# Performance work log

Measured on AMD Instinct MI355X. Metric: run time of the kernel, lower is better.

## Reference

```python
import jax, jax.numpy as jnp
import numpy as np

NUM_HEADS = 16
ROPE_THETA = 10000.0


def _rope_tables(T, head_dim, dtype=jnp.float32):
    # Standard rotate-half RoPE tables: [T, head_dim]
    half = head_dim // 2
    inv_freq = 1.0 / (ROPE_THETA ** (jnp.arange(0, half, dtype=jnp.float32) / half))
    ang = jnp.arange(T, dtype=jnp.float32)[:, None] * inv_freq[None, :]  # [T, half]
    cos = jnp.concatenate([jnp.cos(ang), jnp.cos(ang)], axis=-1).astype(dtype)
    sin = jnp.concatenate([jnp.sin(ang), jnp.sin(ang)], axis=-1).astype(dtype)
    return cos, sin


def _apply_rope(x, cos, sin):
    # x: [B, T, H, D]; cos/sin: [T, D]
    D = x.shape[-1]
    x1, x2 = x[..., : D // 2], x[..., D // 2 :]
    rotated = jnp.concatenate([-x2, x1], axis=-1)
    return x * cos[None, :, None, :] + rotated * sin[None, :, None, :]


def setup_inputs() -> dict:
    key = jax.random.key(0)
    k1, k2, k3 = jax.random.split(key, 3)
    B, T, C = 4, 2048, 2048
    x = jax.random.normal(k1, (B, T, C), dtype=jnp.float32)
    w_attn = jax.random.normal(k2, (C, 3 * C), dtype=jnp.float32) * 0.02
    w_proj = jax.random.normal(k3, (C, C), dtype=jnp.float32) * 0.02
    return {"x": x, "w_attn": w_attn, "w_proj": w_proj}


def reference(x, w_attn, w_proj):
    B, T, C = x.shape
    H = NUM_HEADS
    D = C // H

    qkv = x @ w_attn                         # [B, T, 3C]
    q, k, v = jnp.split(qkv, 3, axis=-1)
    q = q.reshape(B, T, H, D)
    k = k.reshape(B, T, H, D)
    v = v.reshape(B, T, H, D)

    cos, sin = _rope_tables(T, D, x.dtype)
    q = _apply_rope(q, cos, sin)
    k = _apply_rope(k, cos, sin)

    # causal SDPA, heads-first layout [B, H, T, D]
    scale = 1.0 / jnp.sqrt(jnp.asarray(D, dtype=x.dtype))
    scores = jnp.einsum("bqhd,bkhd->bhqk", q, k) * scale  # [B, H, T, T]
    causal = jnp.tril(jnp.ones((T, T), dtype=bool))
    scores = jnp.where(causal[None, None], scores, jnp.finfo(scores.dtype).min)
    attn = jax.nn.softmax(scores, axis=-1)
    y = jnp.einsum("bhqk,bkhd->bqhd", attn, v).reshape(B, T, C)
    return y @ w_proj
```

## Files before the change

kernel.cpp:

```cpp
#include <hip/hip_runtime.h>

typedef __bf16 bf16;
typedef __bf16 bf16x8 __attribute__((ext_vector_type(8)));
typedef __bf16 bf16x4 __attribute__((ext_vector_type(4)));
typedef __bf16 bf16x2 __attribute__((ext_vector_type(2)));
typedef float floatx4 __attribute__((ext_vector_type(4)));
typedef float floatx16 __attribute__((ext_vector_type(16)));

#define NB 4
#define NT 2048
#define NC 2048
#define NH 16
#define ND 128
#define QKS 4096

__device__ __forceinline__ void load_lds16(const void* gptr, void* ldsptr) {
  __builtin_amdgcn_global_load_lds(
      (const __attribute__((address_space(1))) unsigned int*)gptr,
      (__attribute__((address_space(3))) unsigned int*)ldsptr, 16, 0, 0);
}

__device__ __forceinline__ unsigned pack2(float a, float b) {
  bf16x2 v;
  v[0] = (bf16)a; v[1] = (bf16)b;
  return __builtin_bit_cast(unsigned, v);
}

__global__ __launch_bounds__(256) void cast_f32_bf16(const float* __restrict__ in,
                                                     bf16* __restrict__ out) {
  const int i = blockIdx.x * 256 + threadIdx.x;
  const float4 v = ((const float4*)in)[i];
  bf16x4 o;
  o[0] = (bf16)v.x; o[1] = (bf16)v.y; o[2] = (bf16)v.z; o[3] = (bf16)v.w;
  ((bf16x4*)out)[i] = o;
}

__global__ __launch_bounds__(256) void transpose_cast(const float* __restrict__ in,
                                                      bf16* __restrict__ out,
                                                      int R, int Cc) {
  __shared__ float tile[128][65];
  const int r0 = blockIdx.y * 128, c0 = blockIdx.x * 64;
  const int rr = threadIdx.x >> 6, cc = threadIdx.x & 63;
#pragma unroll
  for (int i = 0; i < 32; ++i)
    tile[rr + i * 4][cc] = in[(size_t)(r0 + rr + i * 4) * Cc + c0 + cc];
  __syncthreads();
  const int rv = threadIdx.x & 63, halfr = (threadIdx.x >> 6) & 1, crh = threadIdx.x >> 7;
#pragma unroll
  for (int i = 0; i < 32; ++i) {
    const int cr = crh * 32 + i;
    out[(size_t)(c0 + cr) * R + r0 + halfr * 64 + rv] = (bf16)tile[halfr * 64 + rv][cr];
  }
}

__device__ __forceinline__ void stage_half(bf16* lds, const bf16* __restrict__ g,
                                           int row0, int k0, int h, int K,
                                           int w, int l) {
#pragma unroll
  for (int i = 0; i < 2; ++i) {
    const int fb = h * 1024 + w * 128 + i * 64;
    const int f = fb + l;
    const int r = f >> 3, cs = f & 7, c = cs ^ (r & 7);
    load_lds16(g + (size_t)(row0 + r) * K + k0 + c * 8, lds + fb * 8);
  }
}

template <int EPI, typename OutT>
__global__ __launch_bounds__(512, 2) void gemm_bt(const bf16* __restrict__ A,
                                                  const bf16* __restrict__ Bt,
                                                  OutT* __restrict__ C,
                                                  bf16* __restrict__ qk,
                                                  bf16* __restrict__ vt,
                                                  int M, int N, int K, int NTX) {
  __shared__ bf16 smem[65536];
  __shared__ float invf_s[64];
  const int tid = threadIdx.x;
  const int w = tid >> 6, l = tid & 63, quad = l >> 4, l16 = l & 15;
  const int wm = w >> 2, wn = w & 3;

  const int cpx = gridDim.x >> 3;
  const int orig = blockIdx.x;
  const int wgid = (orig & 7) * cpx + (orig >> 3);
  const int per = 8 * NTX;
  const int band = wgid / per, rem = wgid - band * per;
  const int by = band * 8 + (rem & 7), bx = rem >> 3;
  const int m0 = by * 256, n0 = bx * 256;

  if (EPI == 1 && tid < 64)
    invf_s[tid] = exp2f(-(float)tid * 0.20762050593046014f);

  const int KT = K >> 6;

  const int sw = l16 & 7;
  const int aoff0 = (wm * 128 + l16) * 64 + ((0 + quad) ^ sw) * 8;
  const int aoff1 = (wm * 128 + l16) * 64 + ((4 + quad) ^ sw) * 8;
  const int boff0 = (wn * 64 + l16) * 64 + ((0 + quad) ^ sw) * 8;
  const int boff1 = (wn * 64 + l16) * 64 + ((4 + quad) ^ sw) * 8;

  const floatx4 fzero = {0.f, 0.f, 0.f, 0.f};
  floatx4 acc[8][4];
#pragma unroll
  for (int i = 0; i < 8; ++i)
#pragma unroll
    for (int j = 0; j < 4; ++j) acc[i][j] = fzero;

  bf16x8 af[2][2][2];
  bf16x8 bfr[2][4];

  {
    stage_half(smem, A, m0, 0, 0, K, w, l);
    stage_half(smem, A, m0, 0, 1, K, w, l);
    stage_half(smem + 16384, Bt, n0, 0, 0, K, w, l);
    stage_half(smem + 16384, Bt, n0, 0, 1, K, w, l);
    asm volatile("s_waitcnt vmcnt(0)" ::: "memory");
    __builtin_amdgcn_sched_barrier(0);
    __builtin_amdgcn_s_barrier();
    __builtin_amdgcn_sched_barrier(0);
#pragma unroll
    for (int mr = 0; mr < 2; ++mr) {
      af[0][mr][0] = *(const bf16x8*)(smem + aoff0 + mr * 1024);
      af[0][mr][1] = *(const bf16x8*)(smem + aoff1 + mr * 1024);
    }
#pragma unroll
    for (int ni = 0; ni < 4; ++ni) {
      bfr[0][ni] = *(const bf16x8*)(smem + 16384 + boff0 + ni * 1024);
      bfr[1][ni] = *(const bf16x8*)(smem + 16384 + boff1 + ni * 1024);
    }
  }

#pragma unroll 1
  for (int t = 0; t < KT; ++t) {
    bf16* cur = smem + ((t & 1) << 15);
    bf16* nxt = smem + (((t + 1) & 1) << 15);

#pragma unroll
    for (int p = 0; p < 4; ++p) {
      if (p < 3) {
#pragma unroll
        for (int mr = 0; mr < 2; ++mr) {
          af[(p + 1) & 1][mr][0] =
              *(const bf16x8*)(cur + aoff0 + ((p + 1) * 32 + mr * 16) * 64);
          af[(p + 1) & 1][mr][1] =
              *(const bf16x8*)(cur + aoff1 + ((p + 1) * 32 + mr * 16) * 64);
        }
        if (p == 0 && t + 1 < KT) {
          stage_half(nxt + 16384, Bt, n0, (t + 1) * 64, 0, K, w, l);
          stage_half(nxt + 16384, Bt, n0, (t + 1) * 64, 1, K, w, l);
        }
        if (p == 1 && t + 1 < KT) {
          stage_half(nxt, A, m0, (t + 1) * 64, 0, K, w, l);
          stage_half(nxt, A, m0, (t + 1) * 64, 1, K, w, l);
        }
        __builtin_amdgcn_sched_barrier(0);
        __builtin_amdgcn_s_barrier();
        asm volatile("s_waitcnt lgkmcnt(4)" ::: "memory");
        __builtin_amdgcn_sched_barrier(0);
      } else {
        asm volatile("s_waitcnt vmcnt(0)" ::: "memory");
        __builtin_amdgcn_sched_barrier(0);
        __builtin_amdgcn_s_barrier();
        __builtin_amdgcn_sched_barrier(0);
        if (t + 1 < KT) {
#pragma unroll
          for (int mr = 0; mr < 2; ++mr) {
            af[0][mr][0] = *(const bf16x8*)(nxt + aoff0 + mr * 1024);
            af[0][mr][1] = *(const bf16x8*)(nxt + aoff1 + mr * 1024);
          }
          asm volatile("s_waitcnt lgkmcnt(4)" ::: "memory");
        } else {
          asm volatile("s_waitcnt lgkmcnt(0)" ::: "memory");
        }
        __builtin_amdgcn_sched_barrier(0);
      }

      __builtin_amdgcn_s_setprio(1);
#pragma unroll
      for (int mr = 0; mr < 2; ++mr)
#pragma unroll
        for (int ks = 0; ks < 2; ++ks)
#pragma unroll
          for (int ni = 0; ni < 4; ++ni)
            acc[p * 2 + mr][ni] = __builtin_amdgcn_mfma_f32_16x16x32_bf16(
                af[p & 1][mr][ks], bfr[ks][ni], acc[p * 2 + mr][ni], 0, 0, 0);
      __builtin_amdgcn_s_setprio(0);
      __builtin_amdgcn_sched_barrier(0);

      if (p == 3 && t + 1 < KT) {
#pragma unroll
        for (int ni = 0; ni < 4; ++ni) {
          bfr[0][ni] = *(const bf16x8*)(nxt + 16384 + boff0 + ni * 1024);
          bfr[1][ni] = *(const bf16x8*)(nxt + 16384 + boff1 + ni * 1024);
        }
        __builtin_amdgcn_sched_barrier(0);
      }
      __builtin_amdgcn_s_barrier();
    }
  }

  if constexpr (EPI == 0) {
#pragma unroll
    for (int mi = 0; mi < 8; ++mi)
#pragma unroll
      for (int ni = 0; ni < 4; ++ni) {
        const int row = m0 + wm * 128 + mi * 16 + quad * 4;
        const int col = n0 + wn * 64 + ni * 16 + l16;
#pragma unroll
        for (int r = 0; r < 4; ++r)
          C[(size_t)(row + r) * N + col] = (OutT)acc[mi][ni][r];
      }
  } else {
    bf16* Tl = smem;
#pragma unroll 1
    for (int q = 0; q < 2; ++q) {
      if ((wn >> 1) == q) {
        bf16* Tg = Tl + wm * (128 * 130);
#pragma unroll
        for (int mi = 0; mi < 8; ++mi)
#pragma unroll
          for (int ni = 0; ni < 4; ++ni) {
            const int rl = mi * 16 + quad * 4;
            const int cl = (wn & 1) * 64 + ni * 16 + l16;
#pragma unroll
            for (int r = 0; r < 4; ++r)
              Tg[(rl + r) * 130 + cl] = (bf16)acc[mi][ni][r];
          }
      }
      __syncthreads();

      const int g = tid >> 8, t8 = tid & 255;
      const int m0q = m0 + g * 128, n0q = n0 + q * 128;
      bf16* Tq = Tl + g * (128 * 130);
      const int nt = n0q >> 7;
      if (nt < 32) {
        const int r = t8 >> 1, hd = t8 & 1;
        const float tt = (float)((m0q & (NT - 1)) + r);
        bf16* dst = qk + (size_t)(m0q + r) * QKS + n0q;
#pragma unroll
        for (int j8 = 0; j8 < 2; ++j8) {
          const int d0 = hd * 32 + j8 * 16;
          bf16x8 lo[2], hi[2];
#pragma unroll
          for (int half8 = 0; half8 < 2; ++half8) {
#pragma unroll
            for (int jj = 0; jj < 8; ++jj) {
              const int d = d0 + half8 * 8 + jj;
              const float x1 = (float)Tq[r * 130 + d];
              const float x2 = (float)Tq[r * 130 + d + 64];
              float s, c;
              __sincosf(tt * invf_s[d], &s, &c);
              lo[half8][jj] = (bf16)(x1 * c - x2 * s);
              hi[half8][jj] = (bf16)(x2 * c + x1 * s);
            }
            *(bf16x8*)(dst + d0 + half8 * 8) = lo[half8];
            *(bf16x8*)(dst + d0 + half8 * 8 + 64) = hi[half8];
          }
        }
      } else {
        const int h = nt - 32;
        const int b = m0q >> 11;
        const int t0 = m0q & (NT - 1);
        const int vbase = (b * NH + h) * ND;
#pragma unroll
        for (int ii = 0; ii < 8; ++ii) {
          const int dd = (t8 >> 4) + ii * 16;
          const int ch = t8 & 15;
          bf16x8 o;
#pragma unroll
          for (int j = 0; j < 8; ++j) o[j] = Tq[(ch * 8 + j) * 130 + dd];
          *(bf16x8*)(vt + (size_t)(vbase + dd) * NT + t0 + ch * 8) = o;
        }
      }
      __syncthreads();
    }
  }
}

__global__ __launch_bounds__(256) void attn_kernel(const bf16* __restrict__ qk,
                                                   const bf16* __restrict__ vt,
                                                   bf16* __restrict__ y) {
  __shared__ bf16 Ks[2][64 * 128];
  __shared__ bf16 Vs[2][128 * 64];

  const int pair = blockIdx.x, h = blockIdx.y, b = blockIdx.z;
  const int tid = threadIdx.x;
  const int w = tid >> 6, l = tid & 63, half = l >> 5, l32 = l & 31;
  const float SCL = 0.08838834764831845f * 1.4426950408889634f;

#pragma unroll 1
  for (int pi = 0; pi < 2; ++pi) {
    const int qt = pi ? (15 - pair) : pair;
    const int q0 = qt * 128;
    const int ntiles = qt * 2 + 2;
    const int qg = q0 + w * 32 + l32;

    bf16x8 aq[8];
#pragma unroll
    for (int ks = 0; ks < 8; ++ks)
      aq[ks] = *(const bf16x8*)(qk + (size_t)(b * NT + qg) * QKS + h * ND + ks * 16 + half * 8);

    floatx16 acc[4];
#pragma unroll
    for (int ni = 0; ni < 4; ++ni)
#pragma unroll
      for (int r = 0; r < 16; ++r) acc[ni][r] = 0.f;
    float mold = -3.0e38f, lsum = 0.f;

    {
#pragma unroll
      for (int i = 0; i < 4; ++i) {
        const int fb = i * 256 + w * 64, f = fb + l;
        { const int r = f >> 4, cs = f & 15, c = cs ^ (r & 15);
          load_lds16(qk + (size_t)(b * NT + r) * QKS + NC + h * ND + c * 8, &Ks[0][fb * 8]); }
        { const int r = f >> 3, cs = f & 7, c = cs ^ (r & 7);
          load_lds16(vt + ((size_t)((b * NH + h) * ND + r)) * NT + c * 8, &Vs[0][fb * 8]); }
      }
    }

#pragma unroll 1
    for (int it = 0; it < ntiles; ++it) {
      const int kv0 = it * 64;
      const int buf = it & 1;
      __syncthreads();

      if (it + 1 < ntiles) {
        const int kvn = kv0 + 64, nb = buf ^ 1;
#pragma unroll
        for (int i = 0; i < 4; ++i) {
          const int fb = i * 256 + w * 64, f = fb + l;
          { const int r = f >> 4, cs = f & 15, c = cs ^ (r & 15);
            load_lds16(qk + (size_t)(b * NT + kvn + r) * QKS + NC + h * ND + c * 8, &Ks[nb][fb * 8]); }
          { const int r = f >> 3, cs = f & 7, c = cs ^ (r & 7);
            load_lds16(vt + ((size_t)((b * NH + h) * ND + r)) * NT + kvn + c * 8, &Vs[nb][fb * 8]); }
        }
      }

      if (kv0 <= q0 + w * 32 + 31) {
        floatx16 st[2];
#pragma unroll
        for (int ki = 0; ki < 2; ++ki)
#pragma unroll
          for (int r = 0; r < 16; ++r) st[ki][r] = 0.f;
#pragma unroll
        for (int ks = 0; ks < 8; ++ks) {
          const int slot = (ks * 2 + half) ^ (l32 & 15);
#pragma unroll
          for (int ki = 0; ki < 2; ++ki) {
            const bf16x8 ak = *(const bf16x8*)(&Ks[buf][(ki * 32 + l32) * 128 + slot * 8]);
            st[ki] = __builtin_amdgcn_mfma_f32_32x32x16_bf16(ak, aq[ks], st[ki], 0, 0, 0);
          }
        }

        float mx = -3.0e38f;
        if (kv0 + 63 > q0 + w * 32) {
#pragma unroll
          for (int ki = 0; ki < 2; ++ki)
#pragma unroll
            for (int r = 0; r < 16; ++r) {
              const int kg = kv0 + ki * 32 + (r & 3) + 8 * (r >> 2) + 4 * half;
              float s = st[ki][r] * SCL;
              s = (kg > qg) ? -3.0e38f : s;
              st[ki][r] = s;
              mx = fmaxf(mx, s);
            }
        } else {
#pragma unroll
          for (int ki = 0; ki < 2; ++ki)
#pragma unroll
            for (int r = 0; r < 16; ++r) {
              const float s = st[ki][r] * SCL;
              st[ki][r] = s;
              mx = fmaxf(mx, s);
            }
        }
        mx = fmaxf(mx, __shfl_xor(mx, 32));

        const float mnew = fmaxf(mold, mx);
        const float al = exp2f(mold - mnew);
        float rs = 0.f;
#pragma unroll
        for (int ki = 0; ki < 2; ++ki)
#pragma unroll
          for (int r = 0; r < 16; ++r) {
            const float p = exp2f(st[ki][r] - mnew);
            st[ki][r] = p;
            rs += p;
          }
        rs += __shfl_xor(rs, 32);
        lsum = lsum * al + rs;
        mold = mnew;
#pragma unroll
        for (int ni = 0; ni < 4; ++ni)
#pragma unroll
          for (int r = 0; r < 16; ++r) acc[ni][r] *= al;

        unsigned pk[2][8];
#pragma unroll
        for (int ki = 0; ki < 2; ++ki)
#pragma unroll
          for (int d = 0; d < 8; ++d)
            pk[ki][d] = pack2(st[ki][2 * d], st[ki][2 * d + 1]);
        bf16x8 bp[4];
#pragma unroll
        for (int s = 0; s < 4; ++s) {
          const int ki = s >> 1, o = (s & 1) * 4;
          const unsigned a0 = pk[ki][o], a1 = pk[ki][o + 1], a2 = pk[ki][o + 2], a3 = pk[ki][o + 3];
          const unsigned s0 = (unsigned)__shfl_xor((int)a0, 32);
          const unsigned s1 = (unsigned)__shfl_xor((int)a1, 32);
          const unsigned s2 = (unsigned)__shfl_xor((int)a2, 32);
          const unsigned s3 = (unsigned)__shfl_xor((int)a3, 32);
          uint4 dw;
          dw.x = half ? s2 : a0;
          dw.y = half ? s3 : a1;
          dw.z = half ? a2 : s0;
          dw.w = half ? a3 : s1;
          bp[s] = __builtin_bit_cast(bf16x8, dw);
        }

#pragma unroll
        for (int ni = 0; ni < 4; ++ni) {
          const int rv = ni * 32 + l32;
#pragma unroll
          for (int s = 0; s < 4; ++s) {
            const int slot = (s * 2 + half) ^ (l32 & 7);
            const bf16x8 av = *(const bf16x8*)(&Vs[buf][rv * 64 + slot * 8]);
            acc[ni] = __builtin_amdgcn_mfma_f32_32x32x16_bf16(av, bp[s], acc[ni], 0, 0, 0);
          }
        }
      }
    }

    const float inv = 1.f / lsum;
    const size_t orow = (size_t)(b * NT + qg) * NC + h * ND;
#pragma unroll
    for (int ni = 0; ni < 4; ++ni)
#pragma unroll
      for (int rg = 0; rg < 4; ++rg) {
        bf16x4 o;
#pragma unroll
        for (int j = 0; j < 4; ++j) o[j] = (bf16)(acc[ni][rg * 4 + j] * inv);
        *(bf16x4*)(y + orow + ni * 32 + rg * 8 + half * 4) = o;
      }
    __syncthreads();
  }
}

extern "C" void kernel_launch(void* const* d_in, const int* in_sizes, int n_in,
                              void* d_out, int out_size, void* d_ws, size_t ws_size,
                              hipStream_t stream) {
  const float* x      = (const float*)d_in[0];
  const float* w_attn = (const float*)d_in[1];
  const float* w_proj = (const float*)d_in[2];
  float* out = (float*)d_out;
  char* ws = (char*)d_ws;

  bf16* qk  = (bf16*)(ws);
  bf16* vt  = (bf16*)(ws + 67108864);
  bf16* xb  = (bf16*)(ws + 100663296);
  bf16* wab = (bf16*)(ws + 134217728);
  bf16* y   = wab;
  bf16* wpb = (bf16*)(ws + 167772160);

  cast_f32_bf16<<<dim3(16384), dim3(256), 0, stream>>>(x, xb);
  transpose_cast<<<dim3(96, 16), dim3(256), 0, stream>>>(w_attn, wab, 2048, 6144);
  transpose_cast<<<dim3(32, 16), dim3(256), 0, stream>>>(w_proj, wpb, 2048, 2048);
  gemm_bt<1, float><<<dim3(768), dim3(512), 0, stream>>>(xb, wab, (float*)nullptr, qk, vt,
                                                         8192, 6144, 2048, 24);
  attn_kernel<<<dim3(8, 16, 4), dim3(256), 0, stream>>>(qk, vt, y);
  gemm_bt<0, float><<<dim3(256), dim3(512), 0, stream>>>(y, wpb, out, nullptr, nullptr,
                                                         8192, 2048, 2048, 8);
}
```

Before: 631.3 us.

## Switch GEMM inner loop to 32x32x16 MFMA with precomputed staging pointers

Replaces the 16x16x32 bf16 MFMA tiling with 32x32x16 MFMA, so each wave holds 4x2 floatx16 accumulators and loads fragments with a new lane mapping and matching epilogue index math. Global-to-LDS staging pointers are precomputed once and advanced by 64 each K step, instead of recomputing addresses in stage_half. The larger MFMA shape cuts instruction count and LDS fragment reads per flop. The new register layout changes register pressure and LDS bank patterns in the epilogue.

```diff
diff --git a/kernel.cpp b/kernel.cpp
--- a/kernel.cpp
+++ b/kernel.cpp
@@ -50,18 +50,6 @@
   for (int i = 0; i < 32; ++i) {
     const int cr = crh * 32 + i;
     out[(size_t)(c0 + cr) * R + r0 + halfr * 64 + rv] = (bf16)tile[halfr * 64 + rv][cr];
-  }
-}
-
-__device__ __forceinline__ void stage_half(bf16* lds, const bf16* __restrict__ g,
-                                           int row0, int k0, int h, int K,
-                                           int w, int l) {
-#pragma unroll
-  for (int i = 0; i < 2; ++i) {
-    const int fb = h * 1024 + w * 128 + i * 64;
-    const int f = fb + l;
-    const int r = f >> 3, cs = f & 7, c = cs ^ (r & 7);
-    load_lds16(g + (size_t)(row0 + r) * K + k0 + c * 8, lds + fb * 8);
   }
 }
 
@@ -75,7 +63,7 @@
   __shared__ bf16 smem[65536];
   __shared__ float invf_s[64];
   const int tid = threadIdx.x;
-  const int w = tid >> 6, l = tid & 63, quad = l >> 4, l16 = l & 15;
+  const int w = tid >> 6, l = tid & 63, l32 = l & 31, hi = l >> 5;
   const int wm = w >> 2, wn = w & 3;
 
   const int cpx = gridDim.x >> 3;
@@ -91,41 +79,59 @@
 
   const int KT = K >> 6;
 
-  const int sw = l16 & 7;
-  const int aoff0 = (wm * 128 + l16) * 64 + ((0 + quad) ^ sw) * 8;
-  const int aoff1 = (wm * 128 + l16) * 64 + ((4 + quad) ^ sw) * 8;
-  const int boff0 = (wn * 64 + l16) * 64 + ((0 + quad) ^ sw) * 8;
-  const int boff1 = (wn * 64 + l16) * 64 + ((4 + quad) ^ sw) * 8;
-
-  const floatx4 fzero = {0.f, 0.f, 0.f, 0.f};
-  floatx4 acc[8][4];
-#pragma unroll
-  for (int i = 0; i < 8; ++i)
-#pragma unroll
-    for (int j = 0; j < 4; ++j) acc[i][j] = fzero;
-
-  bf16x8 af[2][2][2];
+  const int sw = l32 & 7;
+  int aoff[4], boff[2][4];
+#pragma unroll
+  for (int ks = 0; ks < 4; ++ks) {
+    aoff[ks] = (wm * 128 + l32) * 64 + (((ks * 2 + hi) ^ sw) * 8);
+#pragma unroll
+    for (int ns = 0; ns < 2; ++ns)
+      boff[ns][ks] = (wn * 64 + ns * 32 + l32) * 64 + (((ks * 2 + hi) ^ sw) * 8);
+  }
+
+  floatx16 acc[4][2];
+#pragma unroll
+  for (int i = 0; i < 4; ++i)
+#pragma unroll
+    for (int j = 0; j < 2; ++j)
+#pragma unroll
+      for (int r = 0; r < 16; ++r) acc[i][j][r] = 0.f;
+
+  bf16x8 af[2][4];
   bf16x8 bfr[2][4];
 
+  const bf16* a_src[4];
+  const bf16* b_src[4];
+  int ldsoff[4];
+#pragma unroll
+  for (int j = 0; j < 4; ++j) {
+    const int h = j >> 1, i = j & 1;
+    const int fb = h * 1024 + w * 128 + i * 64;
+    const int f = fb + l;
+    const int r = f >> 3, cs = f & 7, c = cs ^ (r & 7);
+    ldsoff[j] = fb * 8;
+    a_src[j] = A + (size_t)(m0 + r) * K + c * 8;
+    b_src[j] = Bt + (size_t)(n0 + r) * K + c * 8;
+  }
+
   {
-    stage_half(smem, A, m0, 0, 0, K, w, l);
-    stage_half(smem, A, m0, 0, 1, K, w, l);
-    stage_half(smem + 16384, Bt, n0, 0, 0, K, w, l);
-    stage_half(smem + 16384, Bt, n0, 0, 1, K, w, l);
+#pragma unroll
+    for (int j = 0; j < 4; ++j) load_lds16(a_src[j], smem + ldsoff[j]);
+#pragma unroll
+    for (int j = 0; j < 4; ++j) load_lds16(b_src[j], smem + 16384 + ldsoff[j]);
+#pragma unroll
+    for (int j = 0; j < 4; ++j) { a_src[j] += 64; b_src[j] += 64; }
     asm volatile("s_waitcnt vmcnt(0)" ::: "memory");
     __builtin_amdgcn_sched_barrier(0);
     __builtin_amdgcn_s_barrier();
     __builtin_amdgcn_sched_barrier(0);
 #pragma unroll
-    for (int mr = 0; mr < 2; ++mr) {
-      af[0][mr][0] = *(const bf16x8*)(smem + aoff0 + mr * 1024);
-      af[0][mr][1] = *(const bf16x8*)(smem + aoff1 + mr * 1024);
-    }
-#pragma unroll
-    for (int ni = 0; ni < 4; ++ni) {
-      bfr[0][ni] = *(const bf16x8*)(smem + 16384 + boff0 + ni * 1024);
-      bfr[1][ni] = *(const bf16x8*)(smem + 16384 + boff1 + ni * 1024);
-    }
+    for (int ks = 0; ks < 4; ++ks) af[0][ks] = *(const bf16x8*)(smem + aoff[ks]);
+#pragma unroll
+    for (int ns = 0; ns < 2; ++ns)
+#pragma unroll
+      for (int ks = 0; ks < 4; ++ks)
+        bfr[ns][ks] = *(const bf16x8*)(smem + 16384 + boff[ns][ks]);
   }
 
 #pragma unroll 1
@@ -137,19 +143,20 @@
     for (int p = 0; p < 4; ++p) {
       if (p < 3) {
 #pragma unroll
-        for (int mr = 0; mr < 2; ++mr) {
-          af[(p + 1) & 1][mr][0] =
-              *(const bf16x8*)(cur + aoff0 + ((p + 1) * 32 + mr * 16) * 64);
-          af[(p + 1) & 1][mr][1] =
-              *(const bf16x8*)(cur + aoff1 + ((p + 1) * 32 + mr * 16) * 64);
-        }
+        for (int ks = 0; ks < 4; ++ks)
+          af[(p + 1) & 1][ks] =
+              *(const bf16x8*)(cur + aoff[ks] + (p + 1) * 2048);
         if (p == 0 && t + 1 < KT) {
-          stage_half(nxt + 16384, Bt, n0, (t + 1) * 64, 0, K, w, l);
-          stage_half(nxt + 16384, Bt, n0, (t + 1) * 64, 1, K, w, l);
+#pragma unroll
+          for (int j = 0; j < 4; ++j) load_lds16(b_src[j], nxt + 16384 + ldsoff[j]);
+#pragma unroll
+          for (int j = 0; j < 4; ++j) b_src[j] += 64;
         }
         if (p == 1 && t + 1 < KT) {
-          stage_half(nxt, A, m0, (t + 1) * 64, 0, K, w, l);
-          stage_half(nxt, A, m0, (t + 1) * 64, 1, K, w, l);
+#pragma unroll
+          for (int j = 0; j < 4; ++j) load_lds16(a_src[j], nxt + ldsoff[j]);
+#pragma unroll
+          for (int j = 0; j < 4; ++j) a_src[j] += 64;
         }
         __builtin_amdgcn_sched_barrier(0);
         __builtin_amdgcn_s_barrier();
@@ -162,10 +169,8 @@
         __builtin_amdgcn_sched_barrier(0);
         if (t + 1 < KT) {
 #pragma unroll
-          for (int mr = 0; mr < 2; ++mr) {
-            af[0][mr][0] = *(const bf16x8*)(nxt + aoff0 + mr * 1024);
-            af[0][mr][1] = *(const bf16x8*)(nxt + aoff1 + mr * 1024);
-          }
+          for (int ks = 0; ks < 4; ++ks)
+            af[0][ks] = *(const bf16x8*)(nxt + aoff[ks]);
           asm volatile("s_waitcnt lgkmcnt(4)" ::: "memory");
         } else {
           asm volatile("s_waitcnt lgkmcnt(0)" ::: "memory");
@@ -175,22 +180,20 @@
 
       __builtin_amdgcn_s_setprio(1);
 #pragma unroll
-      for (int mr = 0; mr < 2; ++mr)
-#pragma unroll
-        for (int ks = 0; ks < 2; ++ks)
-#pragma unroll
-          for (int ni = 0; ni < 4; ++ni)
-            acc[p * 2 + mr][ni] = __builtin_amdgcn_mfma_f32_16x16x32_bf16(
-                af[p & 1][mr][ks], bfr[ks][ni], acc[p * 2 + mr][ni], 0, 0, 0);
+      for (int ks = 0; ks < 4; ++ks)
+#pragma unroll
+        for (int ns = 0; ns < 2; ++ns)
+          acc[p][ns] = __builtin_amdgcn_mfma_f32_32x32x16_bf16(
+              af[p & 1][ks], bfr[ns][ks], acc[p][ns], 0, 0, 0);
       __builtin_amdgcn_s_setprio(0);
       __builtin_amdgcn_sched_barrier(0);
 
       if (p == 3 && t + 1 < KT) {
 #pragma unroll
-        for (int ni = 0; ni < 4; ++ni) {
-          bfr[0][ni] = *(const bf16x8*)(nxt + 16384 + boff0 + ni * 1024);
-          bfr[1][ni] = *(const bf16x8*)(nxt + 16384 + boff1 + ni * 1024);
-        }
+        for (int ns = 0; ns < 2; ++ns)
+#pragma unroll
+          for (int ks = 0; ks < 4; ++ks)
+            bfr[ns][ks] = *(const bf16x8*)(nxt + 16384 + boff[ns][ks]);
         __builtin_amdgcn_sched_barrier(0);
       }
       __builtin_amdgcn_s_barrier();
@@ -199,14 +202,15 @@
 
   if constexpr (EPI == 0) {
 #pragma unroll
-    for (int mi = 0; mi < 8; ++mi)
-#pragma unroll
-      for (int ni = 0; ni < 4; ++ni) {
-        const int row = m0 + wm * 128 + mi * 16 + quad * 4;
-        const int col = n0 + wn * 64 + ni * 16 + l16;
-#pragma unroll
-        for (int r = 0; r < 4; ++r)
-          C[(size_t)(row + r) * N + col] = (OutT)acc[mi][ni][r];
+    for (int ms = 0; ms < 4; ++ms)
+#pragma unroll
+      for (int ns = 0; ns < 2; ++ns) {
+        const int col = n0 + wn * 64 + ns * 32 + l32;
+#pragma unroll
+        for (int r = 0; r < 16; ++r) {
+          const int row = m0 + wm * 128 + ms * 32 + (r & 3) + 8 * (r >> 2) + 4 * hi;
+          C[(size_t)row * N + col] = (OutT)acc[ms][ns][r];
+        }
       }
   } else {
     bf16* Tl = smem;
@@ -215,14 +219,15 @@
       if ((wn >> 1) == q) {
         bf16* Tg = Tl + wm * (128 * 130);
 #pragma unroll
-        for (int mi = 0; mi < 8; ++mi)
-#pragma unroll
-          for (int ni = 0; ni < 4; ++ni) {
-            const int rl = mi * 16 + quad * 4;
-            const int cl = (wn & 1) * 64 + ni * 16 + l16;
-#pragma unroll
-            for (int r = 0; r < 4; ++r)
-              Tg[(rl + r) * 130 + cl] = (bf16)acc[mi][ni][r];
+        for (int ms = 0; ms < 4; ++ms)
+#pragma unroll
+          for (int ns = 0; ns < 2; ++ns) {
+            const int cl = (wn & 1) * 64 + ns * 32 + l32;
+#pragma unroll
+            for (int r = 0; r < 16; ++r) {
+              const int rl = ms * 32 + (r & 3) + 8 * (r >> 2) + 4 * hi;
+              Tg[rl * 130 + cl] = (bf16)acc[ms][ns][r];
+            }
           }
       }
       __syncthreads();
@@ -238,7 +243,7 @@
 #pragma unroll
         for (int j8 = 0; j8 < 2; ++j8) {
           const int d0 = hd * 32 + j8 * 16;
-          bf16x8 lo[2], hi[2];
+          bf16x8 lo[2], hi2[2];
 #pragma unroll
           for (int half8 = 0; half8 < 2; ++half8) {
 #pragma unroll
@@ -249,10 +254,10 @@
               float s, c;
               __sincosf(tt * invf_s[d], &s, &c);
               lo[half8][jj] = (bf16)(x1 * c - x2 * s);
-              hi[half8][jj] = (bf16)(x2 * c + x1 * s);
+              hi2[half8][jj] = (bf16)(x2 * c + x1 * s);
             }
             *(bf16x8*)(dst + d0 + half8 * 8) = lo[half8];
-            *(bf16x8*)(dst + d0 + half8 * 8 + 64) = hi[half8];
+            *(bf16x8*)(dst + d0 + half8 * 8 + 64) = hi2[half8];
           }
         }
       } else {
```

New measurement: 638.4 us. No clear change (+1.1%).
